# Kernel tuning notes

Measured on AMD Instinct MI355X. Metric: run time of the kernel, lower is better.

## Reference

```python
import jax, jax.numpy as jnp
import numpy as np

N_NODES = 100000
N_EDGES = 3200000
IN_CH = 256
OUT_CH = 1


def setup_inputs() -> dict:
    key = jax.random.key(0)
    ks = jax.random.split(key, 8)
    x = jax.random.normal(ks[0], (N_NODES, IN_CH), dtype=jnp.float32)
    edge_index = jax.random.randint(ks[1], (2, N_EDGES), 0, N_NODES, dtype=jnp.int64 if jax.config.jax_enable_x64 else jnp.int32)
    s_in = 1.0 / np.sqrt(IN_CH)
    Wq = jax.random.uniform(ks[2], (IN_CH, OUT_CH), jnp.float32, -s_in, s_in)
    bq = jax.random.uniform(ks[3], (OUT_CH,), jnp.float32, -s_in, s_in)
    Wk = jax.random.uniform(ks[4], (IN_CH, OUT_CH), jnp.float32, -s_in, s_in)
    bk = jax.random.uniform(ks[5], (OUT_CH,), jnp.float32, -s_in, s_in)
    Wv = jax.random.uniform(ks[6], (IN_CH, IN_CH), jnp.float32, -s_in, s_in)
    bv = jax.random.uniform(ks[7], (IN_CH,), jnp.float32, -s_in, s_in)
    return {"x": x, "edge_index": edge_index, "Wq": Wq, "bq": bq,
            "Wk": Wk, "bk": bk, "Wv": Wv, "bv": bv}


def reference(x, edge_index, Wq, bq, Wk, bk, Wv, bv):
    num_nodes = x.shape[0]
    q = x @ Wq + bq                       # [N, out_ch]
    k = x @ Wk + bk                       # [N, out_ch]
    v = x @ Wv + bv                       # [N, in_ch]
    row, col = edge_index[0], edge_index[1]
    # edge attention logits: gather + dot over out_ch
    att = jnp.sum(q[row] * k[col], axis=-1)          # [E]
    att = jax.nn.leaky_relu(att, negative_slope=0.2)
    att = jax.nn.softmax(att, axis=0)                # softmax over ALL edges (dim=0)
    # scatter-add edge attention to source nodes
    attention_weights = jax.ops.segment_sum(att, row, num_segments=num_nodes)  # [N]
    graph_emb = jnp.sum(attention_weights[:, None] * v, axis=0)                # [in_ch]
    return graph_emb, attention_weights
```

## Files before the change

kernel.cpp:

```cpp
#include <hip/hip_runtime.h>

#define N_NODES 100000
#define N_EDGES 3200000
#define CH 256

#define GRID_QK 1563
#define GRID_POOL 512
#define YCOPY 16

#define NR 8
#define RANGE 12500
#define SL 64
#define EPS 50000
#define QEPS 12500
#define GP 391

#define OFF_TOTAL 0
#define OFF_PTOT  16
#define OFF_YU16  528
#define OFF_Q     4624
#define OFF_K     104624
#define OFF_AWU   204624
#define OFF_PART  304624

__global__ __launch_bounds__(256) void k_qk(const float* __restrict__ x,
                                            const float* __restrict__ Wq,
                                            const float* __restrict__ bq,
                                            const float* __restrict__ Wk,
                                            const float* __restrict__ bk,
                                            float* __restrict__ q,
                                            float* __restrict__ k,
                                            float* __restrict__ yu16) {
    int t = threadIdx.x;
    if (blockIdx.x < 16) yu16[blockIdx.x * 256 + t] = 0.0f;
    int w = t >> 6, lane = t & 63;
    int g = lane >> 4, seg = lane & 15;
    float4 wq4[4], wk4[4];
    #pragma unroll
    for (int j = 0; j < 4; ++j) {
        wq4[j] = ((const float4*)Wq)[seg + 16 * j];
        wk4[j] = ((const float4*)Wk)[seg + 16 * j];
    }
    float bqs = bq[0], bks = bk[0];
    int base = blockIdx.x * 64 + w * 16 + g;
    #pragma unroll
    for (int i = 0; i < 4; ++i) {
        int n = base + i * 4;
        if (n < N_NODES) {
            const float4* xr = (const float4*)(x + (size_t)n * CH);
            float dq = 0.0f, dk = 0.0f;
            #pragma unroll
            for (int j = 0; j < 4; ++j) {
                float4 xv = xr[seg + 16 * j];
                dq = fmaf(xv.x, wq4[j].x, fmaf(xv.y, wq4[j].y,
                     fmaf(xv.z, wq4[j].z, fmaf(xv.w, wq4[j].w, dq))));
                dk = fmaf(xv.x, wk4[j].x, fmaf(xv.y, wk4[j].y,
                     fmaf(xv.z, wk4[j].z, fmaf(xv.w, wk4[j].w, dk))));
            }
            dq += __shfl_down(dq, 8); dq += __shfl_down(dq, 4);
            dq += __shfl_down(dq, 2); dq += __shfl_down(dq, 1);
            dk += __shfl_down(dk, 8); dk += __shfl_down(dk, 4);
            dk += __shfl_down(dk, 2); dk += __shfl_down(dk, 1);
            if (seg == 0) { q[n] = dq + bqs; k[n] = dk + bks; }
        }
    }
}

__global__ __launch_bounds__(1024) void k_acc(const int* __restrict__ ei,
                                              const float* __restrict__ q,
                                              const float* __restrict__ k,
                                              float* __restrict__ partial) {
    __shared__ float acc[RANGE];
    int t = threadIdx.x;
    int xcd = blockIdx.x & 7;
    int inner = blockIdx.x >> 3;
    int r = inner & 7;
    int s = (inner >> 3) * 8 + xcd;
    for (int i = t; i < RANGE; i += 1024) acc[i] = 0.0f;
    __syncthreads();
    int r0 = r * RANGE;
    const int4* r4p = (const int4*)ei + s * QEPS;
    const int4* c4p = (const int4*)(ei + N_EDGES) + s * QEPS;
    for (int i4 = t; i4 < QEPS; i4 += 1024) {
        int4 rv = r4p[i4];
        int4 cv = c4p[i4];
        unsigned o0 = (unsigned)(rv.x - r0);
        unsigned o1 = (unsigned)(rv.y - r0);
        unsigned o2 = (unsigned)(rv.z - r0);
        unsigned o3 = (unsigned)(rv.w - r0);
        if (o0 < RANGE) {
            float v = q[rv.x] * k[cv.x];
            atomicAdd(&acc[o0], __expf(fmaxf(v, 0.2f * v)));
        }
        if (o1 < RANGE) {
            float v = q[rv.y] * k[cv.y];
            atomicAdd(&acc[o1], __expf(fmaxf(v, 0.2f * v)));
        }
        if (o2 < RANGE) {
            float v = q[rv.z] * k[cv.z];
            atomicAdd(&acc[o2], __expf(fmaxf(v, 0.2f * v)));
        }
        if (o3 < RANGE) {
            float v = q[rv.w] * k[cv.w];
            atomicAdd(&acc[o3], __expf(fmaxf(v, 0.2f * v)));
        }
    }
    __syncthreads();
    float* dst = partial + ((size_t)r * SL + s) * RANGE;
    for (int i = t; i < RANGE; i += 1024) dst[i] = acc[i];
}

__global__ __launch_bounds__(256) void k_fold(const float* __restrict__ partial,
                                              float* __restrict__ awu,
                                              float* __restrict__ ptot) {
    int t = threadIdx.x;
    int n = blockIdx.x * 256 + t;
    float s = 0.0f;
    if (n < N_NODES) {
        int r = n / RANGE, off = n % RANGE;
        const float* p = partial + (size_t)r * SL * RANGE + off;
        #pragma unroll 8
        for (int g = 0; g < SL; ++g) s += p[(size_t)g * RANGE];
        awu[n] = s;
    }
    float rsum = s;
    #pragma unroll
    for (int off = 32; off; off >>= 1) rsum += __shfl_down(rsum, off);
    __shared__ float sm[4];
    if ((t & 63) == 0) sm[t >> 6] = rsum;
    __syncthreads();
    if (t == 0) ptot[blockIdx.x] = sm[0] + sm[1] + sm[2] + sm[3];
}

__global__ __launch_bounds__(256) void k_pool(const float* __restrict__ x,
                                              const float* __restrict__ awu,
                                              const float* __restrict__ ptot,
                                              float* __restrict__ totalp,
                                              float* __restrict__ yu16,
                                              float* __restrict__ aw_out) {
    int t = threadIdx.x, s = t >> 6, g = t & 63;
    float ts = ptot[t] + ((t + 256 < GP) ? ptot[t + 256] : 0.0f);
    #pragma unroll
    for (int off = 32; off; off >>= 1) ts += __shfl_down(ts, off);
    __shared__ float sm[4];
    __shared__ float tot;
    if (g == 0) sm[s] = ts;
    __syncthreads();
    if (t == 0) {
        tot = sm[0] + sm[1] + sm[2] + sm[3];
        if (blockIdx.x == 0) totalp[0] = tot;
    }
    __syncthreads();
    float inv = 1.0f / tot;

    const float4* X4 = (const float4*)x;
    float4 acc = make_float4(0.f, 0.f, 0.f, 0.f);
    for (int base = blockIdx.x * 8; base < N_NODES; base += GRID_POOL * 8) {
        float a0 = awu[base + s];
        float a1 = awu[base + 4 + s];
        float4 x0 = X4[(size_t)(base + s) * 64 + g];
        float4 x1 = X4[(size_t)(base + 4 + s) * 64 + g];
        acc.x = fmaf(a0, x0.x, acc.x); acc.y = fmaf(a0, x0.y, acc.y);
        acc.z = fmaf(a0, x0.z, acc.z); acc.w = fmaf(a0, x0.w, acc.w);
        acc.x = fmaf(a1, x1.x, acc.x); acc.y = fmaf(a1, x1.y, acc.y);
        acc.z = fmaf(a1, x1.z, acc.z); acc.w = fmaf(a1, x1.w, acc.w);
    }
    __shared__ float4 tmp4[4][64];
    tmp4[s][g] = acc;
    __syncthreads();
    const float* tmp = (const float*)tmp4;
    float sum = tmp[0 * 256 + t] + tmp[1 * 256 + t] + tmp[2 * 256 + t] + tmp[3 * 256 + t];
    atomicAdd(&yu16[(blockIdx.x & (YCOPY - 1)) * 256 + t], sum);
    for (int i = blockIdx.x * 256 + t; i < N_NODES; i += GRID_POOL * 256)
        aw_out[i] = awu[i] * inv;
}

__global__ __launch_bounds__(256) void k_final(const float* __restrict__ yu16,
                                               const float* __restrict__ totalp,
                                               const float* __restrict__ Wv,
                                               const float* __restrict__ bv,
                                               float* __restrict__ out) {
    __shared__ float ysh[256];
    __shared__ float red[256];
    int t = threadIdx.x;
    float inv = 1.0f / totalp[0];
    float yv = 0.0f;
    #pragma unroll
    for (int j = 0; j < YCOPY; ++j) yv += yu16[j * 256 + t];
    ysh[t] = yv * inv;
    __syncthreads();
    int c = blockIdx.x * 32 + (t & 31), rg = t >> 5;
    float acc = 0.0f;
    #pragma unroll
    for (int j = 0; j < 32; ++j) {
        int kk = rg * 32 + j;
        acc = fmaf(ysh[kk], Wv[(size_t)kk * CH + c], acc);
    }
    red[t] = acc;
    __syncthreads();
    if (t < 32) {
        float sv = 0.0f;
        #pragma unroll
        for (int j = 0; j < 8; ++j) sv += red[j * 32 + t];
        out[blockIdx.x * 32 + t] = sv + bv[blockIdx.x * 32 + t];
    }
}

extern "C" void kernel_launch(void* const* d_in, const int* in_sizes, int n_in,
                              void* d_out, int out_size, void* d_ws, size_t ws_size,
                              hipStream_t stream) {
    const float* x  = (const float*)d_in[0];
    const int*   ei = (const int*)d_in[1];
    const float* Wq = (const float*)d_in[2];
    const float* bq = (const float*)d_in[3];
    const float* Wk = (const float*)d_in[4];
    const float* bk = (const float*)d_in[5];
    const float* Wv = (const float*)d_in[6];
    const float* bv = (const float*)d_in[7];
    float* out = (float*)d_out;
    float* ws  = (float*)d_ws;

    float* totalp  = ws + OFF_TOTAL;
    float* ptot    = ws + OFF_PTOT;
    float* yu16    = ws + OFF_YU16;
    float* q       = ws + OFF_Q;
    float* k       = ws + OFF_K;
    float* awu     = ws + OFF_AWU;
    float* partial = ws + OFF_PART;

    hipLaunchKernelGGL(k_qk, dim3(GRID_QK), dim3(256), 0, stream,
                       x, Wq, bq, Wk, bk, q, k, yu16);
    hipLaunchKernelGGL(k_acc, dim3(NR * SL), dim3(1024), 0, stream,
                       ei, q, k, partial);
    hipLaunchKernelGGL(k_fold, dim3(GP), dim3(256), 0, stream,
                       partial, awu, ptot);
    hipLaunchKernelGGL(k_pool, dim3(GRID_POOL), dim3(256), 0, stream,
                       x, awu, ptot, totalp, yu16, out + CH);
    hipLaunchKernelGGL(k_final, dim3(8), dim3(256), 0, stream,
                       yu16, totalp, Wv, bv, out);
}
```

Before: 245.3 us.

## Precompute per-edge exp logits in a separate kernel before range accumulation

```diff
diff --git a/kernel.cpp b/kernel.cpp
--- a/kernel.cpp
+++ b/kernel.cpp
@@ -5,6 +5,7 @@
 #define CH 256
 
 #define GRID_QK 1563
+#define GRID_EX 3125
 #define GRID_POOL 512
 #define YCOPY 16
 
@@ -21,7 +22,8 @@
 #define OFF_Q     4624
 #define OFF_K     104624
 #define OFF_AWU   204624
-#define OFF_PART  304624
+#define OFF_EX    304624
+#define OFF_PART  3504624
 
 __global__ __launch_bounds__(256) void k_qk(const float* __restrict__ x,
                                             const float* __restrict__ Wq,
@@ -66,9 +68,26 @@
     }
 }
 
+__global__ __launch_bounds__(256) void k_ex(const int* __restrict__ ei,
+                                            const float* __restrict__ q,
+                                            const float* __restrict__ k,
+                                            float* __restrict__ ex) {
+    int i0 = (blockIdx.x * 256 + threadIdx.x) * 4;
+    const int4 r4 = *(const int4*)(ei + i0);
+    const int4 c4 = *(const int4*)(ei + N_EDGES + i0);
+    float q0 = q[r4.x], q1 = q[r4.y], q2 = q[r4.z], q3 = q[r4.w];
+    float k0 = k[c4.x], k1 = k[c4.y], k2 = k[c4.z], k3 = k[c4.w];
+    float v0 = q0 * k0, v1 = q1 * k1, v2 = q2 * k2, v3 = q3 * k3;
+    float4 e;
+    e.x = __expf(fmaxf(v0, 0.2f * v0));
+    e.y = __expf(fmaxf(v1, 0.2f * v1));
+    e.z = __expf(fmaxf(v2, 0.2f * v2));
+    e.w = __expf(fmaxf(v3, 0.2f * v3));
+    *(float4*)(ex + i0) = e;
+}
+
 __global__ __launch_bounds__(1024) void k_acc(const int* __restrict__ ei,
-                                              const float* __restrict__ q,
-                                              const float* __restrict__ k,
+                                              const float* __restrict__ ex,
                                               float* __restrict__ partial) {
     __shared__ float acc[RANGE];
     int t = threadIdx.x;
@@ -80,30 +99,18 @@
     __syncthreads();
     int r0 = r * RANGE;
     const int4* r4p = (const int4*)ei + s * QEPS;
-    const int4* c4p = (const int4*)(ei + N_EDGES) + s * QEPS;
+    const float4* e4p = (const float4*)ex + s * QEPS;
     for (int i4 = t; i4 < QEPS; i4 += 1024) {
         int4 rv = r4p[i4];
-        int4 cv = c4p[i4];
+        float4 ev = e4p[i4];
         unsigned o0 = (unsigned)(rv.x - r0);
         unsigned o1 = (unsigned)(rv.y - r0);
         unsigned o2 = (unsigned)(rv.z - r0);
         unsigned o3 = (unsigned)(rv.w - r0);
-        if (o0 < RANGE) {
-            float v = q[rv.x] * k[cv.x];
-            atomicAdd(&acc[o0], __expf(fmaxf(v, 0.2f * v)));
-        }
-        if (o1 < RANGE) {
-            float v = q[rv.y] * k[cv.y];
-            atomicAdd(&acc[o1], __expf(fmaxf(v, 0.2f * v)));
-        }
-        if (o2 < RANGE) {
-            float v = q[rv.z] * k[cv.z];
-            atomicAdd(&acc[o2], __expf(fmaxf(v, 0.2f * v)));
-        }
-        if (o3 < RANGE) {
-            float v = q[rv.w] * k[cv.w];
-            atomicAdd(&acc[o3], __expf(fmaxf(v, 0.2f * v)));
-        }
+        if (o0 < RANGE) atomicAdd(&acc[o0], ev.x);
+        if (o1 < RANGE) atomicAdd(&acc[o1], ev.y);
+        if (o2 < RANGE) atomicAdd(&acc[o2], ev.z);
+        if (o3 < RANGE) atomicAdd(&acc[o3], ev.w);
     }
     __syncthreads();
     float* dst = partial + ((size_t)r * SL + s) * RANGE;
@@ -226,12 +233,15 @@
     float* q       = ws + OFF_Q;
     float* k       = ws + OFF_K;
     float* awu     = ws + OFF_AWU;
+    float* ex      = ws + OFF_EX;
     float* partial = ws + OFF_PART;
 
     hipLaunchKernelGGL(k_qk, dim3(GRID_QK), dim3(256), 0, stream,
                        x, Wq, bq, Wk, bk, q, k, yu16);
+    hipLaunchKernelGGL(k_ex, dim3(GRID_EX), dim3(256), 0, stream,
+                       ei, q, k, ex);
     hipLaunchKernelGGL(k_acc, dim3(NR * SL), dim3(1024), 0, stream,
-                       ei, q, k, partial);
+                       ei, ex, partial);
     hipLaunchKernelGGL(k_fold, dim3(GP), dim3(256), 0, stream,
                        partial, awu, ptot);
     hipLaunchKernelGGL(k_pool, dim3(GRID_POOL), dim3(256), 0, stream,
```

Result: slower. 253.8 us (+3.5%).
